# Optimization experiments

Measured on AMD Instinct MI355X. Metric: run time of the kernel, lower is better.

Reference implementation:

```python
import jax, jax.numpy as jnp
import numpy as np

N = 160000   # total nodes
G = 800      # total graphs (B * 50)
NPG = 200    # nodes per graph
E = 1280000  # total edges (avg degree 8)
B = 16       # proteins
K = 2        # TAGConv hops
IN_F = 31
HID = 64


def setup_inputs() -> dict:
    key = jax.random.key(0)
    ks = jax.random.split(key, 16)
    s = 0.1
    x = jax.random.normal(ks[0], (N, IN_F), jnp.float32)
    src = jax.random.randint(ks[1], (E,), 0, N, jnp.int32)
    dst = jax.random.randint(ks[2], (E,), 0, N, jnp.int32)
    node2graph = jnp.repeat(jnp.arange(G, dtype=jnp.int32), NPG)
    W0 = jax.random.normal(ks[3], (IN_F * (K + 1), HID), jnp.float32) * s
    b0 = jax.random.normal(ks[4], (HID,), jnp.float32) * s
    W1 = jax.random.normal(ks[5], (HID * (K + 1), HID), jnp.float32) * s
    b1 = jax.random.normal(ks[6], (HID,), jnp.float32) * s
    W2 = jax.random.normal(ks[7], (HID * (K + 1), HID), jnp.float32) * s
    b2 = jax.random.normal(ks[8], (HID,), jnp.float32) * s
    W3 = jax.random.normal(ks[9], (HID * (K + 1), HID), jnp.float32) * s
    b3 = jax.random.normal(ks[10], (HID,), jnp.float32) * s
    Wg = jax.random.normal(ks[11], (HID, 1), jnp.float32) * s
    bg = jax.random.normal(ks[12], (1,), jnp.float32) * s
    return dict(x=x, src=src, dst=dst, node2graph=node2graph,
                W0=W0, b0=b0, W1=W1, b1=b1, W2=W2, b2=b2, W3=W3, b3=b3,
                Wg=Wg, bg=bg)


def reference(x, src, dst, node2graph, W0, b0, W1, b1, W2, b2, W3, b3, Wg, bg):
    # symmetric normalization: norm = in_degree^{-1/2}, clamped at 1 (DGL TAGConv)
    deg = jax.ops.segment_sum(jnp.ones((E,), x.dtype), dst, num_segments=N)
    norm = jax.lax.rsqrt(jnp.clip(deg, 1.0))[:, None]  # [N,1]

    def tag_conv(h, W, b):
        hops = [h]
        for _ in range(K):
            h = norm * jax.ops.segment_sum((h * norm)[src], dst, num_segments=N)
            hops.append(h)
        return jnp.concatenate(hops, axis=-1) @ W + b

    h = x
    for W, b in ((W0, b0), (W1, b1), (W2, b2), (W3, b3)):
        h = jax.nn.relu(tag_conv(h, W, b))

    # GlobalAttentionPooling: per-graph softmax over gate logits, weighted sum
    gate = h @ Wg + bg  # [N,1]
    gmax = jax.ops.segment_max(gate, node2graph, num_segments=G)  # [G,1]
    e = jnp.exp(gate - gmax[node2graph])
    z = jax.ops.segment_sum(e, node2graph, num_segments=G)
    alpha = e / z[node2graph]
    readout = jax.ops.segment_sum(alpha * h, node2graph, num_segments=G)  # [G,64]
    return readout.reshape(B, 50, HID)
```

## Files before the change

kernel.cpp:

```cpp
#include <hip/hip_runtime.h>

#define NN 160000
#define NE 1280000
#define NG 800
#define NPGR 200
#define INF_ 31
#define HID 64

#define NBUK 256
#define NPBK 625
#define BCAP 6144
#define CHUNK 8192

typedef unsigned short bfu;
typedef __attribute__((ext_vector_type(8))) short short8;
typedef __attribute__((ext_vector_type(4))) float f32x4;

__device__ inline float bflo(unsigned u) { return __uint_as_float(u << 16); }
__device__ inline float bfhi(unsigned u) { return __uint_as_float(u & 0xffff0000u); }
__device__ inline float bfs(bfu s) { return __uint_as_float(((unsigned)s) << 16); }
__device__ inline unsigned f2bf(float x) {
  unsigned u = __float_as_uint(x);
  return (u + 0x7fffu + ((u >> 16) & 1u)) >> 16;
}
__device__ inline unsigned pack2(float a, float b) {
  return f2bf(a) | (f2bf(b) << 16);
}
__device__ inline void unpack8(uint4 v, float* f) {
  f[0] = bflo(v.x); f[1] = bfhi(v.x);
  f[2] = bflo(v.y); f[3] = bfhi(v.y);
  f[4] = bflo(v.z); f[5] = bfhi(v.z);
  f[6] = bflo(v.w); f[7] = bfhi(v.w);
}

__global__ __launch_bounds__(256) void k_pad(const float* __restrict__ x,
                                             bfu* __restrict__ xb) {
  int i = blockIdx.x * 256 + threadIdx.x;
  int n = i >> 5, f = i & 31;
  float v = (f < INF_) ? x[(size_t)n * INF_ + f] : 0.f;
  xb[i] = (bfu)f2bf(v);
}

__global__ __launch_bounds__(256) void k_wfrag(const float* __restrict__ W,
                                               short* __restrict__ Wf) {
  int idx = blockIdx.x * 256 + threadIdx.x;
  int lane = idx & 63, t = (idx >> 6) & 3, step = idx >> 8;
  int col = t * 16 + (lane & 15);
  int kbase = step * 32 + ((lane >> 4) & 3) * 8;
  short8 o;
#pragma unroll
  for (int j = 0; j < 8; ++j)
    o[j] = (short)f2bf(W[(size_t)(kbase + j) * 64 + col]);
  *reinterpret_cast<short8*>(&Wf[(size_t)idx * 8]) = o;
}

__global__ __launch_bounds__(256) void k_wfrag0(const float* __restrict__ W0,
                                                short* __restrict__ Wf) {
  int idx = blockIdx.x * 256 + threadIdx.x;
  int lane = idx & 63, t = (idx >> 6) & 3, step = idx >> 8;
  int col = t * 16 + (lane & 15);
  int kbase = step * 32 + ((lane >> 4) & 3) * 8;
  short8 o;
#pragma unroll
  for (int j = 0; j < 8; ++j) {
    int r = kbase + j, pp = r >> 5, ir = r & 31;
    float v = (ir < INF_) ? W0[(size_t)(pp * INF_ + ir) * 64 + col] : 0.f;
    o[j] = (short)f2bf(v);
  }
  *reinterpret_cast<short8*>(&Wf[(size_t)idx * 8]) = o;
}

__global__ __launch_bounds__(256) void k_gcinit(int* __restrict__ gcur) {
  gcur[threadIdx.x] = threadIdx.x * BCAP;
}

__global__ __launch_bounds__(256) void k_bucket(const int* __restrict__ src,
    const int* __restrict__ dst, int* __restrict__ gcur,
    uint2* __restrict__ buk, int E) {
  __shared__ uint2 stage[CHUNK];
  __shared__ int cnt[NBUK], gbase[NBUK];
  int tid = threadIdx.x;
  int base = blockIdx.x * CHUNK;
  int nch = min(CHUNK, E - base);
  for (int i = tid; i < NBUK; i += 256) cnt[i] = 0;
  __syncthreads();
  for (int i = tid; i < nch; i += 256) {
    int s = src[base + i], d = dst[base + i];
    stage[i] = make_uint2((unsigned)s, (unsigned)d);
    atomicAdd(&cnt[(unsigned)d / NPBK], 1);
  }
  __syncthreads();
  for (int i = tid; i < NBUK; i += 256) {
    gbase[i] = atomicAdd(&gcur[i], cnt[i]);
    cnt[i] = 0;
  }
  __syncthreads();
  for (int i = tid; i < nch; i += 256) {
    uint2 r = stage[i];
    int b = r.y / NPBK;
    int off = atomicAdd(&cnt[b], 1);
    buk[(size_t)gbase[b] + off] = r;
  }
}

__global__ __launch_bounds__(256) void k_count(const uint2* __restrict__ buk,
    const int* __restrict__ gcur, int* __restrict__ deg,
    int* __restrict__ order) {
  __shared__ int cnt[NPBK];
  __shared__ int h64[64], c64[64];
  int b = blockIdx.x, tid = threadIdx.x;
  int nbase = b * NPBK;
  for (int i = tid; i < NPBK; i += 256) cnt[i] = 0;
  if (tid < 64) h64[tid] = 0;
  __syncthreads();
  int n = gcur[b] - b * BCAP;
  const uint2* __restrict__ bp = buk + (size_t)b * BCAP;
  for (int i = tid; i < n; i += 256) atomicAdd(&cnt[bp[i].y - nbase], 1);
  __syncthreads();
  for (int i = tid; i < NPBK; i += 256) {
    int c = cnt[i];
    deg[nbase + i] = c;
    atomicAdd(&h64[min(c, 63)], 1);
  }
  __syncthreads();
  if (tid == 0) {
    int s = 0;
    for (int k = 0; k < 64; ++k) { c64[k] = s; s += h64[k]; }
  }
  __syncthreads();
  for (int i = tid; i < NPBK; i += 256) {
    int pos = atomicAdd(&c64[min(cnt[i], 63)], 1);
    order[nbase + pos] = nbase + i;
  }
}

__global__ __launch_bounds__(256) void k_bscan(const int* __restrict__ gcur,
                                               int* __restrict__ bktoff) {
  __shared__ int sh[256];
  int tid = threadIdx.x;
  sh[tid] = gcur[tid] - tid * BCAP;
  __syncthreads();
  for (int off = 1; off < 256; off <<= 1) {
    int v = (tid >= off) ? sh[tid - off] : 0;
    __syncthreads();
    sh[tid] += v;
    __syncthreads();
  }
  bktoff[tid] = (tid > 0) ? sh[tid - 1] : 0;
}

__global__ __launch_bounds__(256) void k_scat2(const uint2* __restrict__ buk,
    const int* __restrict__ gcur, const int* __restrict__ bktoff,
    const int* __restrict__ deg, int* __restrict__ rp,
    unsigned* __restrict__ csr) {
  __shared__ int cur[NPBK];
  int b = blockIdx.x, tid = threadIdx.x;
  int nbase = b * NPBK;
  if (tid == 0) {
    int s = bktoff[b];
    for (int i = 0; i < NPBK; ++i) {
      cur[i] = s;
      rp[nbase + i] = s;
      s += deg[nbase + i];
    }
    if (b == NBUK - 1) rp[NN] = NE;
  }
  __syncthreads();
  int n = gcur[b] - b * BCAP;
  const uint2* __restrict__ bp = buk + (size_t)b * BCAP;
  for (int i = tid; i < n; i += 256) {
    uint2 r = bp[i];
    int pos = atomicAdd(&cur[r.y - nbase], 1);
    unsigned d = min((unsigned)deg[r.x], 16383u);
    csr[pos] = (d << 18) | r.x;
  }
}

template<int F>
__global__ __launch_bounds__(256) void k_gather(const bfu* __restrict__ hin,
    const int* __restrict__ rp, const unsigned* __restrict__ csr,
    const int* __restrict__ order, bfu* __restrict__ hout) {
  constexpr int LPN = F / 8;
  constexpr int NPB = 256 / LPN;
  int slot = threadIdx.x / LPN;
  int f8 = (threadIdx.x % LPN) * 8;
  int nid = order[blockIdx.x * NPB + slot];
  int beg = rp[nid], end = rp[nid + 1];
  float acc[8] = {0.f, 0.f, 0.f, 0.f, 0.f, 0.f, 0.f, 0.f};
  int e = beg;
  for (; e + 8 <= end; e += 8) {
    unsigned ed[8];
    uint4 v[8];
#pragma unroll
    for (int k = 0; k < 8; ++k) ed[k] = csr[e + k];
#pragma unroll
    for (int k = 0; k < 8; ++k)
      v[k] = *reinterpret_cast<const uint4*>(&hin[(size_t)(ed[k] & 0x3FFFFu) * F + f8]);
#pragma unroll
    for (int k = 0; k < 8; ++k) {
      float f[8];
      unpack8(v[k], f);
      float w = rsqrtf(fmaxf((float)(ed[k] >> 18), 1.0f));
#pragma unroll
      for (int q = 0; q < 8; ++q) acc[q] = fmaf(f[q], w, acc[q]);
    }
  }
  for (; e + 2 <= end; e += 2) {
    unsigned e0 = csr[e], e1 = csr[e + 1];
    uint4 v0 = *reinterpret_cast<const uint4*>(&hin[(size_t)(e0 & 0x3FFFFu) * F + f8]);
    uint4 v1 = *reinterpret_cast<const uint4*>(&hin[(size_t)(e1 & 0x3FFFFu) * F + f8]);
    float f0[8], f1[8];
    unpack8(v0, f0); unpack8(v1, f1);
    float w0 = rsqrtf(fmaxf((float)(e0 >> 18), 1.0f));
    float w1 = rsqrtf(fmaxf((float)(e1 >> 18), 1.0f));
#pragma unroll
    for (int q = 0; q < 8; ++q) {
      acc[q] = fmaf(f0[q], w0, acc[q]);
      acc[q] = fmaf(f1[q], w1, acc[q]);
    }
  }
  if (e < end) {
    unsigned e0 = csr[e];
    uint4 v0 = *reinterpret_cast<const uint4*>(&hin[(size_t)(e0 & 0x3FFFFu) * F + f8]);
    float f0[8];
    unpack8(v0, f0);
    float w0 = rsqrtf(fmaxf((float)(e0 >> 18), 1.0f));
#pragma unroll
    for (int q = 0; q < 8; ++q) acc[q] = fmaf(f0[q], w0, acc[q]);
  }
  float wn = rsqrtf(fmaxf((float)(end - beg), 1.0f));
#pragma unroll
  for (int q = 0; q < 8; ++q) acc[q] *= wn;
  uint4 o;
  o.x = pack2(acc[0], acc[1]);
  o.y = pack2(acc[2], acc[3]);
  o.z = pack2(acc[4], acc[5]);
  o.w = pack2(acc[6], acc[7]);
  *reinterpret_cast<uint4*>(&hout[(size_t)nid * F + f8]) = o;
}

template<int F>
__global__ __launch_bounds__(256) void k_gemm_mfma(const bfu* __restrict__ h0,
    const bfu* __restrict__ h1, const bfu* __restrict__ h2,
    const short* __restrict__ Wf, const float* __restrict__ bias,
    bfu* __restrict__ outb) {
  constexpr int SPP = F / 32;
  int wave = threadIdx.x >> 6, lane = threadIdx.x & 63;
  int quad = lane >> 4, l15 = lane & 15;
  int nb = blockIdx.x * 64 + wave * 16;

  f32x4 acc[4] = {{0.f,0.f,0.f,0.f}, {0.f,0.f,0.f,0.f},
                  {0.f,0.f,0.f,0.f}, {0.f,0.f,0.f,0.f}};
  const bfu* parts[3] = {h0, h1, h2};
#pragma unroll
  for (int p = 0; p < 3; ++p) {
    const bfu* __restrict__ P = parts[p] + (size_t)(nb + l15) * F + quad * 8;
#pragma unroll
    for (int s = 0; s < SPP; ++s) {
      short8 a = *reinterpret_cast<const short8*>(P + s * 32);
      int step = p * SPP + s;
      const short* __restrict__ wb = Wf + ((size_t)step * 4 * 64 + lane) * 8;
#pragma unroll
      for (int t = 0; t < 4; ++t) {
        short8 b = *reinterpret_cast<const short8*>(wb + (size_t)t * 64 * 8);
        acc[t] = __builtin_amdgcn_mfma_f32_16x16x32_bf16(a, b, acc[t], 0, 0, 0);
      }
    }
  }
#pragma unroll
  for (int t = 0; t < 4; ++t) {
    int col = t * 16 + l15;
    float bj = bias[col];
#pragma unroll
    for (int r = 0; r < 4; ++r) {
      int node = nb + quad * 4 + r;
      float v = fmaxf(acc[t][r] + bj, 0.f);
      outb[(size_t)node * 64 + col] = (bfu)f2bf(v);
    }
  }
}

__global__ __launch_bounds__(256) void k_pool(const bfu* __restrict__ h,
    const float* __restrict__ Wg, const float* __restrict__ bg,
    float* __restrict__ out) {
  int g = blockIdx.x;
  int tid = threadIdx.x;
  int lane = tid & 63, w = tid >> 6;
  const bfu* hg = h + (size_t)g * NPGR * HID;
  float wgt = Wg[lane];
  __shared__ float sgate[NPGR];
  __shared__ float sred[256];
  __shared__ float spart[4][64];

  for (int n = w; n < NPGR; n += 4) {
    float v = bfs(hg[(size_t)n * HID + lane]) * wgt;
    for (int off = 32; off > 0; off >>= 1) v += __shfl_down(v, off, 64);
    if (lane == 0) sgate[n] = v + bg[0];
  }
  __syncthreads();

  float m = -INFINITY;
  for (int n = tid; n < NPGR; n += 256) m = fmaxf(m, sgate[n]);
  sred[tid] = m;
  __syncthreads();
  for (int s = 128; s > 0; s >>= 1) {
    if (tid < s) sred[tid] = fmaxf(sred[tid], sred[tid + s]);
    __syncthreads();
  }
  float gmax = sred[0];
  __syncthreads();

  float zp = 0.f;
  for (int n = tid; n < NPGR; n += 256) {
    float e = expf(sgate[n] - gmax);
    sgate[n] = e;
    zp += e;
  }
  sred[tid] = zp;
  __syncthreads();
  for (int s = 128; s > 0; s >>= 1) {
    if (tid < s) sred[tid] += sred[tid + s];
    __syncthreads();
  }
  float z = sred[0];
  __syncthreads();

  float acc = 0.f;
  for (int n = w; n < NPGR; n += 4)
    acc += sgate[n] * bfs(hg[(size_t)n * HID + lane]);
  spart[w][lane] = acc;
  __syncthreads();
  if (w == 0) {
    float t = spart[0][lane] + spart[1][lane] + spart[2][lane] + spart[3][lane];
    out[(size_t)g * HID + lane] = t / z;
  }
}

extern "C" void kernel_launch(void* const* d_in, const int* in_sizes, int n_in,
                              void* d_out, int out_size, void* d_ws, size_t ws_size,
                              hipStream_t stream) {
  const float* x   = (const float*)d_in[0];
  const int*   src = (const int*)d_in[1];
  const int*   dst = (const int*)d_in[2];
  const float* W0 = (const float*)d_in[4];
  const float* b0 = (const float*)d_in[5];
  const float* W1 = (const float*)d_in[6];
  const float* b1 = (const float*)d_in[7];
  const float* W2 = (const float*)d_in[8];
  const float* b2 = (const float*)d_in[9];
  const float* W3 = (const float*)d_in[10];
  const float* b3 = (const float*)d_in[11];
  const float* Wg = (const float*)d_in[12];
  const float* bg = (const float*)d_in[13];
  float* out = (float*)d_out;

  const int N = NN, E = NE;

  char* p = (char*)d_ws;
  unsigned* csr = (unsigned*)p;      p += sizeof(unsigned) * (size_t)E;
  int* deg     = (int*)p;            p += sizeof(int) * (size_t)N;
  int* rp      = (int*)p;            p += sizeof(int) * (size_t)(N + 4);
  int* order   = (int*)p;            p += sizeof(int) * (size_t)N;
  int* gcur    = (int*)p;            p += sizeof(int) * NBUK;
  int* bktoff  = (int*)p;            p += sizeof(int) * NBUK;
  short* Wf0   = (short*)p;          p += sizeof(short) * 768 * 8;
  short* Wf1   = (short*)p;          p += sizeof(short) * 1536 * 8;
  short* Wf2   = (short*)p;          p += sizeof(short) * 1536 * 8;
  short* Wf3   = (short*)p;          p += sizeof(short) * 1536 * 8;
  bfu* xb      = (bfu*)p;            p += sizeof(bfu) * (size_t)N * 32;
  bfu* h1b     = (bfu*)p;            p += sizeof(bfu) * (size_t)N * HID;
  bfu* h2b     = (bfu*)p;            p += sizeof(bfu) * (size_t)N * HID;
  bfu* hAb     = (bfu*)p;            p += sizeof(bfu) * (size_t)N * HID;
  bfu* hBb     = (bfu*)p;            p += sizeof(bfu) * (size_t)N * HID;
  uint2* buk   = (uint2*)hBb;

  k_gcinit<<<1, NBUK, 0, stream>>>(gcur);
  k_bucket<<<(E + CHUNK - 1) / CHUNK, 256, 0, stream>>>(src, dst, gcur, buk, E);
  k_count<<<NBUK, 256, 0, stream>>>(buk, gcur, deg, order);
  k_bscan<<<1, NBUK, 0, stream>>>(gcur, bktoff);
  k_scat2<<<NBUK, 256, 0, stream>>>(buk, gcur, bktoff, deg, rp, csr);

  k_pad<<<(N * 32) / 256, 256, 0, stream>>>(x, xb);
  k_wfrag0<<<3, 256, 0, stream>>>(W0, Wf0);
  k_wfrag<<<6, 256, 0, stream>>>(W1, Wf1);
  k_wfrag<<<6, 256, 0, stream>>>(W2, Wf2);
  k_wfrag<<<6, 256, 0, stream>>>(W3, Wf3);

  k_gather<32><<<N / 64, 256, 0, stream>>>(xb, rp, csr, order, h1b);
  k_gather<32><<<N / 64, 256, 0, stream>>>(h1b, rp, csr, order, h2b);
  k_gemm_mfma<32><<<N / 64, 256, 0, stream>>>(xb, h1b, h2b, Wf0, b0, hAb);

  const short* Wfs[3] = {Wf1, Wf2, Wf3};
  const float* bs[3] = {b1, b2, b3};
  bfu* hin = hAb;
  bfu* hout = hBb;
  for (int l = 0; l < 3; ++l) {
    k_gather<64><<<N / 32, 256, 0, stream>>>(hin, rp, csr, order, h1b);
    k_gather<64><<<N / 32, 256, 0, stream>>>(h1b, rp, csr, order, h2b);
    k_gemm_mfma<64><<<N / 64, 256, 0, stream>>>(hin, h1b, h2b, Wfs[l], bs[l], hout);
    bfu* t = hin; hin = hout; hout = t;
  }

  k_pool<<<NG, 256, 0, stream>>>(hin, Wg, bg, out);
}
```

Measured before the change: 639.2 us.

## Fuse second-hop gather into MFMA GEMM and parallelize CSR row-pointer scan

The second-hop neighbour gather now runs inside the GEMM kernel and writes its results to shared memory, so the h2 buffer is never written to or read back from global memory, and four launches go away. Row pointers in the CSR build are now computed with a block-wide parallel scan instead of a serial loop on one thread. Edge bucketing reads src/dst with vectorized int4 loads, and the pooling kernel stages each graph's features in shared memory. In exchange, the GEMM kernel does irregular gathers with lower parallelism per block, follows the degree order for its A rows, and gets a separate bucket buffer in the workspace.

```diff
diff --git a/kernel.cpp b/kernel.cpp
--- a/kernel.cpp
+++ b/kernel.cpp
@@ -84,10 +84,17 @@
   int nch = min(CHUNK, E - base);
   for (int i = tid; i < NBUK; i += 256) cnt[i] = 0;
   __syncthreads();
-  for (int i = tid; i < nch; i += 256) {
-    int s = src[base + i], d = dst[base + i];
-    stage[i] = make_uint2((unsigned)s, (unsigned)d);
-    atomicAdd(&cnt[(unsigned)d / NPBK], 1);
+  for (int i = tid * 4; i < nch; i += 1024) {
+    int4 s4 = *reinterpret_cast<const int4*>(&src[base + i]);
+    int4 d4 = *reinterpret_cast<const int4*>(&dst[base + i]);
+    stage[i + 0] = make_uint2((unsigned)s4.x, (unsigned)d4.x);
+    stage[i + 1] = make_uint2((unsigned)s4.y, (unsigned)d4.y);
+    stage[i + 2] = make_uint2((unsigned)s4.z, (unsigned)d4.z);
+    stage[i + 3] = make_uint2((unsigned)s4.w, (unsigned)d4.w);
+    atomicAdd(&cnt[(unsigned)d4.x / NPBK], 1);
+    atomicAdd(&cnt[(unsigned)d4.y / NPBK], 1);
+    atomicAdd(&cnt[(unsigned)d4.z / NPBK], 1);
+    atomicAdd(&cnt[(unsigned)d4.w / NPBK], 1);
   }
   __syncthreads();
   for (int i = tid; i < NBUK; i += 256) {
@@ -154,17 +161,26 @@
     const int* __restrict__ deg, int* __restrict__ rp,
     unsigned* __restrict__ csr) {
   __shared__ int cur[NPBK];
+  __shared__ int psum[256];
   int b = blockIdx.x, tid = threadIdx.x;
   int nbase = b * NPBK;
-  if (tid == 0) {
-    int s = bktoff[b];
-    for (int i = 0; i < NPBK; ++i) {
-      cur[i] = s;
-      rp[nbase + i] = s;
-      s += deg[nbase + i];
-    }
-    if (b == NBUK - 1) rp[NN] = NE;
-  }
+  int i0 = tid * 3;
+  int d0 = (i0 + 0 < NPBK) ? deg[nbase + i0 + 0] : 0;
+  int d1 = (i0 + 1 < NPBK) ? deg[nbase + i0 + 1] : 0;
+  int d2 = (i0 + 2 < NPBK) ? deg[nbase + i0 + 2] : 0;
+  psum[tid] = d0 + d1 + d2;
+  __syncthreads();
+  for (int off = 1; off < 256; off <<= 1) {
+    int v = (tid >= off) ? psum[tid - off] : 0;
+    __syncthreads();
+    psum[tid] += v;
+    __syncthreads();
+  }
+  int excl = bktoff[b] + ((tid > 0) ? psum[tid - 1] : 0);
+  if (i0 + 0 < NPBK) { cur[i0 + 0] = excl; rp[nbase + i0 + 0] = excl; excl += d0; }
+  if (i0 + 1 < NPBK) { cur[i0 + 1] = excl; rp[nbase + i0 + 1] = excl; excl += d1; }
+  if (i0 + 2 < NPBK) { cur[i0 + 2] = excl; rp[nbase + i0 + 2] = excl; excl += d2; }
+  if (b == NBUK - 1 && tid == 0) rp[NN] = NE;
   __syncthreads();
   int n = gcur[b] - b * BCAP;
   const uint2* __restrict__ bp = buk + (size_t)b * BCAP;
@@ -174,6 +190,62 @@
     unsigned d = min((unsigned)deg[r.x], 16383u);
     csr[pos] = (d << 18) | r.x;
   }
+}
+
+template<int F>
+__device__ inline uint4 gather_node(const bfu* __restrict__ hin,
+    const unsigned* __restrict__ csr, int beg, int end, int f8) {
+  float acc[8] = {0.f, 0.f, 0.f, 0.f, 0.f, 0.f, 0.f, 0.f};
+  int e = beg;
+  for (; e + 8 <= end; e += 8) {
+    unsigned ed[8];
+    uint4 v[8];
+#pragma unroll
+    for (int k = 0; k < 8; ++k) ed[k] = csr[e + k];
+#pragma unroll
+    for (int k = 0; k < 8; ++k)
+      v[k] = *reinterpret_cast<const uint4*>(&hin[(size_t)(ed[k] & 0x3FFFFu) * F + f8]);
+#pragma unroll
+    for (int k = 0; k < 8; ++k) {
+      float f[8];
+      unpack8(v[k], f);
+      float w = rsqrtf(fmaxf((float)(ed[k] >> 18), 1.0f));
+#pragma unroll
+      for (int q = 0; q < 8; ++q) acc[q] = fmaf(f[q], w, acc[q]);
+    }
+  }
+  for (; e + 2 <= end; e += 2) {
+    unsigned e0 = csr[e], e1 = csr[e + 1];
+    uint4 v0 = *reinterpret_cast<const uint4*>(&hin[(size_t)(e0 & 0x3FFFFu) * F + f8]);
+    uint4 v1 = *reinterpret_cast<const uint4*>(&hin[(size_t)(e1 & 0x3FFFFu) * F + f8]);
+    float f0[8], f1[8];
+    unpack8(v0, f0); unpack8(v1, f1);
+    float w0 = rsqrtf(fmaxf((float)(e0 >> 18), 1.0f));
+    float w1 = rsqrtf(fmaxf((float)(e1 >> 18), 1.0f));
+#pragma unroll
+    for (int q = 0; q < 8; ++q) {
+      acc[q] = fmaf(f0[q], w0, acc[q]);
+      acc[q] = fmaf(f1[q], w1, acc[q]);
+    }
+  }
+  if (e < end) {
+    unsigned e0 = csr[e];
+    uint4 v0 = *reinterpret_cast<const uint4*>(&hin[(size_t)(e0 & 0x3FFFFu) * F + f8]);
+    float f0[8];
+    unpack8(v0, f0);
+    float w0 = rsqrtf(fmaxf((float)(e0 >> 18), 1.0f));
+#pragma unroll
+    for (int q = 0; q < 8; ++q) acc[q] = fmaf(f0[q], w0, acc[q]);
+  }
+  float wn = rsqrtf(fmaxf((float)(end - beg), 1.0f));
+#pragma unroll
+  for (int q = 0; q < 8; ++q) acc[q] *= wn;
+  uint4 o;
+  o.x = pack2(acc[0], acc[1]);
+  o.y = pack2(acc[2], acc[3]);
+  o.z = pack2(acc[4], acc[5]);
+  o.w = pack2(acc[6], acc[7]);
+  return o;
 }
 
 template<int F>
@@ -186,75 +258,47 @@
   int f8 = (threadIdx.x % LPN) * 8;
   int nid = order[blockIdx.x * NPB + slot];
   int beg = rp[nid], end = rp[nid + 1];
-  float acc[8] = {0.f, 0.f, 0.f, 0.f, 0.f, 0.f, 0.f, 0.f};
-  int e = beg;
-  for (; e + 8 <= end; e += 8) {
-    unsigned ed[8];
-    uint4 v[8];
-#pragma unroll
-    for (int k = 0; k < 8; ++k) ed[k] = csr[e + k];
-#pragma unroll
-    for (int k = 0; k < 8; ++k)
-      v[k] = *reinterpret_cast<const uint4*>(&hin[(size_t)(ed[k] & 0x3FFFFu) * F + f8]);
-#pragma unroll
-    for (int k = 0; k < 8; ++k) {
-      float f[8];
-      unpack8(v[k], f);
-      float w = rsqrtf(fmaxf((float)(ed[k] >> 18), 1.0f));
-#pragma unroll
-      for (int q = 0; q < 8; ++q) acc[q] = fmaf(f[q], w, acc[q]);
-    }
-  }
-  for (; e + 2 <= end; e += 2) {
-    unsigned e0 = csr[e], e1 = csr[e + 1];
-    uint4 v0 = *reinterpret_cast<const uint4*>(&hin[(size_t)(e0 & 0x3FFFFu) * F + f8]);
-    uint4 v1 = *reinterpret_cast<const uint4*>(&hin[(size_t)(e1 & 0x3FFFFu) * F + f8]);
-    float f0[8], f1[8];
-    unpack8(v0, f0); unpack8(v1, f1);
-    float w0 = rsqrtf(fmaxf((float)(e0 >> 18), 1.0f));
-    float w1 = rsqrtf(fmaxf((float)(e1 >> 18), 1.0f));
-#pragma unroll
-    for (int q = 0; q < 8; ++q) {
-      acc[q] = fmaf(f0[q], w0, acc[q]);
-      acc[q] = fmaf(f1[q], w1, acc[q]);
-    }
-  }
-  if (e < end) {
-    unsigned e0 = csr[e];
-    uint4 v0 = *reinterpret_cast<const uint4*>(&hin[(size_t)(e0 & 0x3FFFFu) * F + f8]);
-    float f0[8];
-    unpack8(v0, f0);
-    float w0 = rsqrtf(fmaxf((float)(e0 >> 18), 1.0f));
-#pragma unroll
-    for (int q = 0; q < 8; ++q) acc[q] = fmaf(f0[q], w0, acc[q]);
-  }
-  float wn = rsqrtf(fmaxf((float)(end - beg), 1.0f));
-#pragma unroll
-  for (int q = 0; q < 8; ++q) acc[q] *= wn;
-  uint4 o;
-  o.x = pack2(acc[0], acc[1]);
-  o.y = pack2(acc[2], acc[3]);
-  o.z = pack2(acc[4], acc[5]);
-  o.w = pack2(acc[6], acc[7]);
+  uint4 o = gather_node<F>(hin, csr, beg, end, f8);
   *reinterpret_cast<uint4*>(&hout[(size_t)nid * F + f8]) = o;
 }
 
 template<int F>
-__global__ __launch_bounds__(256) void k_gemm_mfma(const bfu* __restrict__ h0,
-    const bfu* __restrict__ h1, const bfu* __restrict__ h2,
+__global__ __launch_bounds__(256) void k_hop2gemm(const bfu* __restrict__ h0,
+    const bfu* __restrict__ h1, const int* __restrict__ rp,
+    const unsigned* __restrict__ csr, const int* __restrict__ order,
     const short* __restrict__ Wf, const float* __restrict__ bias,
     bfu* __restrict__ outb) {
   constexpr int SPP = F / 32;
-  int wave = threadIdx.x >> 6, lane = threadIdx.x & 63;
+  constexpr int LPN = F / 8;
+  constexpr int NPR = 256 / LPN;
+  constexpr int NFB = F / 8;
+  __shared__ uint4 hs[64 * (NFB + 1)];
+
+  int tid = threadIdx.x;
+  int nb = blockIdx.x * 64;
+
+#pragma unroll
+  for (int round = 0; round < 64 / NPR; ++round) {
+    int slot = round * NPR + tid / LPN;
+    int f8 = tid % LPN;
+    int nid = order[nb + slot];
+    int beg = rp[nid], end = rp[nid + 1];
+    uint4 o = gather_node<F>(h1, csr, beg, end, f8 * 8);
+    hs[slot * (NFB + 1) + f8] = o;
+  }
+  __syncthreads();
+
+  int wave = tid >> 6, lane = tid & 63;
   int quad = lane >> 4, l15 = lane & 15;
-  int nb = blockIdx.x * 64 + wave * 16;
+  int aslot = wave * 16 + l15;
+  int anid = order[nb + aslot];
 
   f32x4 acc[4] = {{0.f,0.f,0.f,0.f}, {0.f,0.f,0.f,0.f},
                   {0.f,0.f,0.f,0.f}, {0.f,0.f,0.f,0.f}};
-  const bfu* parts[3] = {h0, h1, h2};
-#pragma unroll
-  for (int p = 0; p < 3; ++p) {
-    const bfu* __restrict__ P = parts[p] + (size_t)(nb + l15) * F + quad * 8;
+  const bfu* parts[2] = {h0, h1};
+#pragma unroll
+  for (int p = 0; p < 2; ++p) {
+    const bfu* __restrict__ P = parts[p] + (size_t)anid * F + quad * 8;
 #pragma unroll
     for (int s = 0; s < SPP; ++s) {
       short8 a = *reinterpret_cast<const short8*>(P + s * 32);
@@ -268,12 +312,23 @@
     }
   }
 #pragma unroll
+  for (int s = 0; s < SPP; ++s) {
+    short8 a = *reinterpret_cast<const short8*>(&hs[aslot * (NFB + 1) + s * 4 + quad]);
+    int step = 2 * SPP + s;
+    const short* __restrict__ wb = Wf + ((size_t)step * 4 * 64 + lane) * 8;
+#pragma unroll
+    for (int t = 0; t < 4; ++t) {
+      short8 b = *reinterpret_cast<const short8*>(wb + (size_t)t * 64 * 8);
+      acc[t] = __builtin_amdgcn_mfma_f32_16x16x32_bf16(a, b, acc[t], 0, 0, 0);
+    }
+  }
+#pragma unroll
   for (int t = 0; t < 4; ++t) {
     int col = t * 16 + l15;
     float bj = bias[col];
 #pragma unroll
     for (int r = 0; r < 4; ++r) {
-      int node = nb + quad * 4 + r;
+      int node = order[nb + wave * 16 + quad * 4 + r];
       float v = fmaxf(acc[t][r] + bj, 0.f);
       outb[(size_t)node * 64 + col] = (bfu)f2bf(v);
     }
@@ -283,17 +338,22 @@
 __global__ __launch_bounds__(256) void k_pool(const bfu* __restrict__ h,
     const float* __restrict__ Wg, const float* __restrict__ bg,
     float* __restrict__ out) {
+  __shared__ uint4 hsl[NPGR * 8];
+  __shared__ float sgate[NPGR];
+  __shared__ float sred[256];
+  __shared__ float spart[4][64];
   int g = blockIdx.x;
   int tid = threadIdx.x;
   int lane = tid & 63, w = tid >> 6;
-  const bfu* hg = h + (size_t)g * NPGR * HID;
+  const uint4* __restrict__ hg4 = reinterpret_cast<const uint4*>(
+      h + (size_t)g * NPGR * HID);
+  for (int i = tid; i < NPGR * 8; i += 256) hsl[i] = hg4[i];
+  __syncthreads();
+  const bfu* hsb = reinterpret_cast<const bfu*>(hsl);
   float wgt = Wg[lane];
-  __shared__ float sgate[NPGR];
-  __shared__ float sred[256];
-  __shared__ float spart[4][64];
 
   for (int n = w; n < NPGR; n += 4) {
-    float v = bfs(hg[(size_t)n * HID + lane]) * wgt;
+    float v = bfs(hsb[n * HID + lane]) * wgt;
     for (int off = 32; off > 0; off >>= 1) v += __shfl_down(v, off, 64);
     if (lane == 0) sgate[n] = v + bg[0];
   }
@@ -327,7 +387,7 @@
 
   float acc = 0.f;
   for (int n = w; n < NPGR; n += 4)
-    acc += sgate[n] * bfs(hg[(size_t)n * HID + lane]);
+    acc += sgate[n] * bfs(hsb[n * HID + lane]);
   spart[w][lane] = acc;
   __syncthreads();
   if (w == 0) {
@@ -369,10 +429,10 @@
   short* Wf3   = (short*)p;          p += sizeof(short) * 1536 * 8;
   bfu* xb      = (bfu*)p;            p += sizeof(bfu) * (size_t)N * 32;
   bfu* h1b     = (bfu*)p;            p += sizeof(bfu) * (size_t)N * HID;
-  bfu* h2b     = (bfu*)p;            p += sizeof(bfu) * (size_t)N * HID;
   bfu* hAb     = (bfu*)p;            p += sizeof(bfu) * (size_t)N * HID;
   bfu* hBb     = (bfu*)p;            p += sizeof(bfu) * (size_t)N * HID;
-  uint2* buk   = (uint2*)hBb;
+  uint2* buk   = (uint2*)p;
+  p += sizeof(uint2) * (size_t)NBUK * BCAP;
 
   k_gcinit<<<1, NBUK, 0, stream>>>(gcur);
   k_bucket<<<(E + CHUNK - 1) / CHUNK, 256, 0, stream>>>(src, dst, gcur, buk, E);
@@ -387,8 +447,8 @@
   k_wfrag<<<6, 256, 0, stream>>>(W3, Wf3);
 
   k_gather<32><<<N / 64, 256, 0, stream>>>(xb, rp, csr, order, h1b);
-  k_gather<32><<<N / 64, 256, 0, stream>>>(h1b, rp, csr, order, h2b);
-  k_gemm_mfma<32><<<N / 64, 256, 0, stream>>>(xb, h1b, h2b, Wf0, b0, hAb);
+  k_hop2gemm<32><<<N / 64, 256, 0, stream>>>(xb, h1b, rp, csr, order,
+                                             Wf0, b0, hAb);
 
   const short* Wfs[3] = {Wf1, Wf2, Wf3};
   const float* bs[3] = {b1, b2, b3};
@@ -396,8 +456,8 @@
   bfu* hout = hBb;
   for (int l = 0; l < 3; ++l) {
     k_gather<64><<<N / 32, 256, 0, stream>>>(hin, rp, csr, order, h1b);
-    k_gather<64><<<N / 32, 256, 0, stream>>>(h1b, rp, csr, order, h2b);
-    k_gemm_mfma<64><<<N / 64, 256, 0, stream>>>(hin, h1b, h2b, Wfs[l], bs[l], hout);
+    k_hop2gemm<64><<<N / 64, 256, 0, stream>>>(hin, h1b, rp, csr, order,
+                                               Wfs[l], bs[l], hout);
     bfu* t = hin; hin = hout; hout = t;
   }
 
```

After: 579.6 us. -9.3%, faster.
